# Kernel optimization log

Measured on AMD Instinct MI355X. Metric: run time of the kernel, lower is better.

## Reference

```python
import jax, jax.numpy as jnp
import numpy as np
from jax import lax

B, S, D, F, E, K = 4, 2048, 2048, 8192, 8, 2


def setup_inputs() -> dict:
    key = jax.random.key(0)
    ks = jax.random.split(key, 4)
    sd = 1.0 / np.sqrt(D)
    sf = 1.0 / np.sqrt(F)
    return {
        "hidden_states": jax.random.normal(ks[0], (B, S, D), dtype=jnp.float32),
        "router_w": jax.random.normal(ks[1], (D, E), dtype=jnp.float32) * sd,
        "w1": jax.random.normal(ks[2], (E, D, F), dtype=jnp.float32) * sd,
        "b1": jnp.zeros((E, F), dtype=jnp.float32),
        "w2": jax.random.normal(ks[3], (E, F, D), dtype=jnp.float32) * sf,
        "b2": jnp.zeros((E, D), dtype=jnp.float32),
        "top_k": K,
    }


def reference(hidden_states, router_w, w1, b1, w2, b2, top_k):
    b, s, d = hidden_states.shape
    x = hidden_states.reshape(-1, d)  # [T, D] flat tokens
    # Router: top-k over expert logits, softmax over the selected logits.
    logits = x @ router_w                      # [T, E]
    top_vals, top_idx = lax.top_k(logits, top_k)  # [T, K]
    scores = jax.nn.softmax(top_vals, axis=-1)    # [T, K]

    out = jnp.zeros_like(x)
    n_experts = w1.shape[0]
    for e in range(n_experts):  # fixed small expert count
        # per-token combine weight for this expert (0 if not routed)
        cw = jnp.sum(jnp.where(top_idx == e, scores, 0.0), axis=-1)  # [T]
        h = jax.nn.gelu(x @ w1[e] + b1[e], approximate=False)        # [T, F]
        out = out + cw[:, None] * (h @ w2[e] + b2[e])                # masked combine
    out = out.reshape(b, s, d)
    return out + hidden_states  # use_residual=True
```

## Files before the change

kernel.cpp:

```cpp
#include <hip/hip_runtime.h>

#define T_TOK 8192
#define DIM   2048
#define FFN   8192
#define NE    8
#define TOPK  2

typedef unsigned short ushort_t;
typedef unsigned short ushort8  __attribute__((ext_vector_type(8)));
typedef unsigned short ushort4v __attribute__((ext_vector_type(4)));
typedef short bf16x8 __attribute__((ext_vector_type(8)));
typedef float f32x4  __attribute__((ext_vector_type(4)));

__device__ __forceinline__ ushort_t f2bf(float f) {
  unsigned int u = __float_as_uint(f);
  u += 0x7FFFu + ((u >> 16) & 1u);
  return (ushort_t)(u >> 16);
}
__device__ __forceinline__ float bf2f(ushort_t u) {
  return __uint_as_float(((unsigned int)u) << 16);
}

__device__ __forceinline__ void gload16(const void* g, void* l) {
  __builtin_amdgcn_global_load_lds((const __attribute__((address_space(1))) void*)g,
                                   (__attribute__((address_space(3))) void*)l, 16, 0, 0);
}

__global__ void k_cast(const float* __restrict__ x, ushort_t* __restrict__ xbf) {
  int i = blockIdx.x * blockDim.x + threadIdx.x;
  float4 v = reinterpret_cast<const float4*>(x)[i];
  ushort4v o;
  o.x = f2bf(v.x); o.y = f2bf(v.y); o.z = f2bf(v.z); o.w = f2bf(v.w);
  reinterpret_cast<ushort4v*>(xbf)[i] = o;
}

#define TT 64
__global__ __launch_bounds__(256) void k_wcvt(const float* __restrict__ in,
                                              ushort_t* __restrict__ outp, int R, int C) {
  __shared__ ushort_t t[TT][TT + 8];
  int e = blockIdx.z;
  const float* src = in + (size_t)e * R * C;
  ushort_t* dst = outp + (size_t)e * R * C;
  int r0 = blockIdx.y * TT, c0 = blockIdx.x * TT;
  int tid = threadIdx.x;
  int rr = tid >> 4;
  int c4 = tid & 15;
#pragma unroll
  for (int i = 0; i < 4; i++) {
    int r = rr + i * 16;
    float4 v = *reinterpret_cast<const float4*>(src + (size_t)(r0 + r) * C + c0 + c4 * 4);
    ushort4v p;
    p.x = f2bf(v.x); p.y = f2bf(v.y); p.z = f2bf(v.z); p.w = f2bf(v.w);
    *reinterpret_cast<ushort4v*>(&t[r][c4 * 4]) = p;
  }
  __syncthreads();
  int c = tid >> 2, rs = tid & 3;
  ushort_t tmp[16];
#pragma unroll
  for (int i = 0; i < 16; i++) tmp[i] = t[rs * 16 + i][c];
  ushort8 v0, v1;
#pragma unroll
  for (int i = 0; i < 8; i++) { v0[i] = tmp[i]; v1[i] = tmp[8 + i]; }
  ushort_t* drow = dst + (size_t)(c0 + c) * R + r0 + rs * 16;
  *reinterpret_cast<ushort8*>(drow) = v0;
  *reinterpret_cast<ushort8*>(drow + 8) = v1;
}

__global__ __launch_bounds__(256) void k_router(
    const float* __restrict__ x, const float* __restrict__ rw,
    int* __restrict__ tidx, float* __restrict__ twt, int* __restrict__ counts) {
  int t = blockIdx.x;
  int tid = threadIdx.x;
  int lane = tid & 63, wave = tid >> 6;
  float acc[NE];
#pragma unroll
  for (int e = 0; e < NE; e++) acc[e] = 0.f;
  const float* xr = x + (size_t)t * DIM;
  for (int d = tid; d < DIM; d += 256) {
    float xv = xr[d];
    const float* r = rw + d * NE;
#pragma unroll
    for (int e = 0; e < NE; e++) acc[e] += xv * r[e];
  }
  __shared__ float wsum[4][NE];
#pragma unroll
  for (int e = 0; e < NE; e++) {
    float v = acc[e];
#pragma unroll
    for (int off = 32; off > 0; off >>= 1) v += __shfl_down(v, off);
    if (lane == 0) wsum[wave][e] = v;
  }
  __syncthreads();
  if (tid == 0) {
    float lg[NE];
#pragma unroll
    for (int e = 0; e < NE; e++) lg[e] = wsum[0][e] + wsum[1][e] + wsum[2][e] + wsum[3][e];
    int i0 = 0; float v0 = lg[0];
#pragma unroll
    for (int e = 1; e < NE; e++) if (lg[e] > v0) { v0 = lg[e]; i0 = e; }
    int i1 = -1; float v1 = -3.4e38f;
#pragma unroll
    for (int e = 0; e < NE; e++) if (e != i0 && lg[e] > v1) { v1 = lg[e]; i1 = e; }
    float e1 = expf(v1 - v0);
    float s = 1.f + e1;
    tidx[t * 2 + 0] = i0; tidx[t * 2 + 1] = i1;
    twt[t * 2 + 0] = 1.f / s; twt[t * 2 + 1] = e1 / s;
    atomicAdd(&counts[i0], 1);
    atomicAdd(&counts[i1], 1);
  }
}

__global__ void k_scan(const int* __restrict__ counts, int* __restrict__ offsets) {
  if (threadIdx.x == 0) {
    int s = 0;
    for (int e = 0; e < NE; e++) { offsets[e] = s; s += counts[e]; }
    offsets[NE] = s;
  }
}

__global__ void k_fill(const int* __restrict__ tidx, const float* __restrict__ twt,
                       const int* __restrict__ offsets, int* __restrict__ cursors,
                       int* __restrict__ ltok, float* __restrict__ lwt, int* __restrict__ ppos) {
  int t = blockIdx.x * blockDim.x + threadIdx.x;
  if (t >= T_TOK) return;
#pragma unroll
  for (int k = 0; k < TOPK; k++) {
    int e = tidx[t * 2 + k];
    int pos = atomicAdd(&cursors[e], 1);
    int p = offsets[e] + pos;
    ltok[p] = t;
    lwt[p] = twt[t * 2 + k];
    ppos[t * 2 + k] = p;
  }
}

#define BM 128
#define BN 128
#define BK 32

__global__ __launch_bounds__(256) void k_gemm1(
    const ushort_t* __restrict__ xbf, const ushort_t* __restrict__ w1t, const float* __restrict__ b1,
    const int* __restrict__ counts, const int* __restrict__ offsets,
    const int* __restrict__ ltok, ushort_t* __restrict__ H) {
  int e = blockIdx.z;
  int cnt = counts[e];
  int row0 = blockIdx.y * BM;
  if (row0 >= cnt) return;
  int base = offsets[e];
  int col0 = blockIdx.x * BN;
  const ushort_t* Bt = w1t + (size_t)e * DIM * FFN;

  __shared__ __align__(16) ushort_t As[BM * BK];
  __shared__ __align__(16) ushort_t Bs[BN * BK];

  int tid = threadIdx.x;
  int wave = tid >> 6, lane = tid & 63;
  int wm = wave >> 1, wn = wave & 1;
  int lm = lane & 15, lg = lane >> 4;

  int srow = tid >> 2, seg = tid & 3;
  const ushort_t* asrc[2]; const ushort_t* bsrc[2];
#pragma unroll
  for (int j = 0; j < 2; j++) {
    int ar = min(row0 + j * 64 + srow, cnt - 1);
    asrc[j] = xbf + (size_t)ltok[base + ar] * DIM + seg * 8;
    bsrc[j] = Bt + (size_t)(col0 + j * 64 + srow) * DIM + seg * 8;
  }
  f32x4 acc[4][4];
#pragma unroll
  for (int m = 0; m < 4; m++)
#pragma unroll
    for (int n = 0; n < 4; n++) acc[m][n] = (f32x4){0.f, 0.f, 0.f, 0.f};

  for (int k0 = 0; k0 < DIM; k0 += BK) {
#pragma unroll
    for (int j = 0; j < 2; j++) {
      gload16(asrc[j] + k0, &As[(j * 256 + wave * 64) * 8]);
      gload16(bsrc[j] + k0, &Bs[(j * 256 + wave * 64) * 8]);
    }
    __syncthreads();
    bf16x8 af[4], bfv[4];
#pragma unroll
    for (int m = 0; m < 4; m++)
      af[m] = *reinterpret_cast<const bf16x8*>(&As[(wm * 64 + m * 16 + lm) * BK + lg * 8]);
#pragma unroll
    for (int n = 0; n < 4; n++)
      bfv[n] = *reinterpret_cast<const bf16x8*>(&Bs[(wn * 64 + n * 16 + lm) * BK + lg * 8]);
#pragma unroll
    for (int m = 0; m < 4; m++)
#pragma unroll
      for (int n = 0; n < 4; n++)
        acc[m][n] = __builtin_amdgcn_mfma_f32_16x16x32_bf16(af[m], bfv[n], acc[m][n], 0, 0, 0);
    __syncthreads();
  }
#pragma unroll
  for (int m = 0; m < 4; m++) {
#pragma unroll
    for (int n = 0; n < 4; n++) {
      int f = col0 + wn * 64 + n * 16 + lm;
      float bias = b1[e * FFN + f];
#pragma unroll
      for (int r = 0; r < 4; r++) {
        int row = row0 + wm * 64 + m * 16 + lg * 4 + r;
        if (row < cnt) {
          float v = acc[m][n][r] + bias;
          float g = 0.5f * v * (1.0f + erff(v * 0.70710678118654752f));
          H[(size_t)(base + row) * FFN + f] = f2bf(g);
        }
      }
    }
  }
}

__global__ __launch_bounds__(256) void k_gemm2(
    const ushort_t* __restrict__ H, const ushort_t* __restrict__ w2t, const float* __restrict__ b2,
    const int* __restrict__ counts, const int* __restrict__ offsets,
    const float* __restrict__ lwt, ushort_t* __restrict__ contrib) {
  int e = blockIdx.z;
  int cnt = counts[e];
  int row0 = blockIdx.y * BM;
  if (row0 >= cnt) return;
  int base = offsets[e];
  int col0 = blockIdx.x * BN;
  const ushort_t* Bt = w2t + (size_t)e * DIM * FFN;

  __shared__ __align__(16) ushort_t As[BM * BK];
  __shared__ __align__(16) ushort_t Bs[BN * BK];

  int tid = threadIdx.x;
  int wave = tid >> 6, lane = tid & 63;
  int wm = wave >> 1, wn = wave & 1;
  int lm = lane & 15, lg = lane >> 4;

  int srow = tid >> 2, seg = tid & 3;
  const ushort_t* asrc[2]; const ushort_t* bsrc[2];
#pragma unroll
  for (int j = 0; j < 2; j++) {
    int ar = min(row0 + j * 64 + srow, cnt - 1);
    asrc[j] = H + (size_t)(base + ar) * FFN + seg * 8;
    bsrc[j] = Bt + (size_t)(col0 + j * 64 + srow) * FFN + seg * 8;
  }
  f32x4 acc[4][4];
#pragma unroll
  for (int m = 0; m < 4; m++)
#pragma unroll
    for (int n = 0; n < 4; n++) acc[m][n] = (f32x4){0.f, 0.f, 0.f, 0.f};

  for (int k0 = 0; k0 < FFN; k0 += BK) {
#pragma unroll
    for (int j = 0; j < 2; j++) {
      gload16(asrc[j] + k0, &As[(j * 256 + wave * 64) * 8]);
      gload16(bsrc[j] + k0, &Bs[(j * 256 + wave * 64) * 8]);
    }
    __syncthreads();
    bf16x8 af[4], bfv[4];
#pragma unroll
    for (int m = 0; m < 4; m++)
      af[m] = *reinterpret_cast<const bf16x8*>(&As[(wm * 64 + m * 16 + lm) * BK + lg * 8]);
#pragma unroll
    for (int n = 0; n < 4; n++)
      bfv[n] = *reinterpret_cast<const bf16x8*>(&Bs[(wn * 64 + n * 16 + lm) * BK + lg * 8]);
#pragma unroll
    for (int m = 0; m < 4; m++)
#pragma unroll
      for (int n = 0; n < 4; n++)
        acc[m][n] = __builtin_amdgcn_mfma_f32_16x16x32_bf16(af[m], bfv[n], acc[m][n], 0, 0, 0);
    __syncthreads();
  }
#pragma unroll
  for (int m = 0; m < 4; m++) {
#pragma unroll
    for (int n = 0; n < 4; n++) {
      int d = col0 + wn * 64 + n * 16 + lm;
      float bias = b2[e * DIM + d];
#pragma unroll
      for (int r = 0; r < 4; r++) {
        int row = row0 + wm * 64 + m * 16 + lg * 4 + r;
        if (row < cnt) {
          float v = (acc[m][n][r] + bias) * lwt[base + row];
          contrib[(size_t)(base + row) * DIM + d] = f2bf(v);
        }
      }
    }
  }
}

__global__ void k_combine(const float* __restrict__ x, const ushort_t* __restrict__ contrib,
                          const int* __restrict__ ppos, float* __restrict__ out) {
  int i = blockIdx.x * blockDim.x + threadIdx.x;
  int t = i / (DIM / 4);
  int dq = i % (DIM / 4);
  int p0 = ppos[t * 2 + 0], p1 = ppos[t * 2 + 1];
  float4 xv = reinterpret_cast<const float4*>(x)[i];
  ushort4v c0 = reinterpret_cast<const ushort4v*>(contrib + (size_t)p0 * DIM)[dq];
  ushort4v c1 = reinterpret_cast<const ushort4v*>(contrib + (size_t)p1 * DIM)[dq];
  float4 o;
  o.x = xv.x + bf2f(c0.x) + bf2f(c1.x);
  o.y = xv.y + bf2f(c0.y) + bf2f(c1.y);
  o.z = xv.z + bf2f(c0.z) + bf2f(c1.z);
  o.w = xv.w + bf2f(c0.w) + bf2f(c1.w);
  reinterpret_cast<float4*>(out)[i] = o;
}

extern "C" void kernel_launch(void* const* d_in, const int* in_sizes, int n_in,
                              void* d_out, int out_size, void* d_ws, size_t ws_size,
                              hipStream_t stream) {
  const float* x  = (const float*)d_in[0];
  const float* rw = (const float*)d_in[1];
  const float* w1 = (const float*)d_in[2];
  const float* b1 = (const float*)d_in[3];
  const float* w2 = (const float*)d_in[4];
  const float* b2 = (const float*)d_in[5];
  float* out = (float*)d_out;
  char* ws = (char*)d_ws;

  const size_t MB = 1u << 20;
  int*   counts  = (int*)(ws);
  int*   offsets = (int*)(ws + 64);
  int*   cursors = (int*)(ws + 128);
  int*   tidx    = (int*)(ws + 1 * MB);
  float* twt     = (float*)(ws + 2 * MB);
  int*   ltok    = (int*)(ws + 3 * MB);
  float* lwt     = (float*)(ws + 4 * MB);
  int*   ppos    = (int*)(ws + 5 * MB);
  ushort_t* xbf     = (ushort_t*)(ws + 8 * MB);
  ushort_t* contrib = (ushort_t*)(ws + 8 * MB);
  ushort_t* Hbuf    = (ushort_t*)(ws + 72 * MB);
  ushort_t* w1t     = (ushort_t*)(ws + 328 * MB);
  ushort_t* w2t     = (ushort_t*)(ws + 328 * MB);
  const size_t NEED = 584 * MB;
  if (ws_size < NEED) {
    hipMemsetAsync(d_out, 0, (size_t)out_size * sizeof(float), stream);
    return;
  }

  hipMemsetAsync(ws, 0, 256, stream);
  k_cast<<<dim3((T_TOK * (size_t)DIM / 4) / 256), 256, 0, stream>>>(x, xbf);
  k_router<<<T_TOK, 256, 0, stream>>>(x, rw, tidx, twt, counts);
  k_scan<<<1, 64, 0, stream>>>(counts, offsets);
  k_fill<<<T_TOK / 256, 256, 0, stream>>>(tidx, twt, offsets, cursors, ltok, lwt, ppos);
  k_wcvt<<<dim3(FFN / TT, DIM / TT, NE), 256, 0, stream>>>(w1, w1t, DIM, FFN);
  k_gemm1<<<dim3(FFN / BN, T_TOK / BM, NE), 256, 0, stream>>>(xbf, w1t, b1, counts, offsets, ltok, Hbuf);
  k_wcvt<<<dim3(DIM / TT, FFN / TT, NE), 256, 0, stream>>>(w2, w2t, FFN, DIM);
  k_gemm2<<<dim3(DIM / BN, T_TOK / BM, NE), 256, 0, stream>>>(Hbuf, w2t, b2, counts, offsets, lwt, contrib);
  k_combine<<<dim3((T_TOK * (size_t)DIM / 4) / 256), 256, 0, stream>>>(x, contrib, ppos, out);
}
```

Measured before the change: 2.193 ms.

## Double-buffer LDS in expert GEMMs, swap grid order, faster GELU erf

Both expert GEMM kernels now use two LDS buffers and prefetch the next K-slice while the MFMAs run on the current one, dropping one barrier per iteration. The grid is transposed so the row tiles of one expert (the empty ones exit early) sit in the fast-varying dimension. s_setprio is raised around the MFMA block and launch bounds ask for 4 blocks per CU. The exact erf in GELU is replaced by the Abramowitz-Stegun polynomial with rcp and expf, cutting epilogue cost but adding about 1e-7 absolute erf error, well below bf16 rounding.

```diff
diff --git a/kernel.cpp b/kernel.cpp
--- a/kernel.cpp
+++ b/kernel.cpp
@@ -24,6 +24,20 @@
 __device__ __forceinline__ void gload16(const void* g, void* l) {
   __builtin_amdgcn_global_load_lds((const __attribute__((address_space(1))) void*)g,
                                    (__attribute__((address_space(3))) void*)l, 16, 0, 0);
+}
+
+__device__ __forceinline__ float gelu_exact(float v) {
+  float s = v * 0.70710678118654752f;
+  float a = fabsf(s);
+  float t = __builtin_amdgcn_rcpf(1.0f + 0.3275911f * a);
+  float p = t * (0.254829592f +
+            t * (-0.284496736f +
+            t * (1.421413741f +
+            t * (-1.453152027f +
+            t * 1.061405429f))));
+  float er = 1.0f - p * __expf(-a * a);
+  er = copysignf(er, s);
+  return 0.5f * v * (1.0f + er);
 }
 
 __global__ void k_cast(const float* __restrict__ x, ushort_t* __restrict__ xbf) {
@@ -138,28 +152,28 @@
 #define BN 128
 #define BK 32
 
-__global__ __launch_bounds__(256) void k_gemm1(
+__global__ __launch_bounds__(256, 4) void k_gemm1(
     const ushort_t* __restrict__ xbf, const ushort_t* __restrict__ w1t, const float* __restrict__ b1,
     const int* __restrict__ counts, const int* __restrict__ offsets,
     const int* __restrict__ ltok, ushort_t* __restrict__ H) {
   int e = blockIdx.z;
   int cnt = counts[e];
-  int row0 = blockIdx.y * BM;
+  int row0 = blockIdx.x * BM;
   if (row0 >= cnt) return;
   int base = offsets[e];
-  int col0 = blockIdx.x * BN;
+  int col0 = blockIdx.y * BN;
   const ushort_t* Bt = w1t + (size_t)e * DIM * FFN;
 
-  __shared__ __align__(16) ushort_t As[BM * BK];
-  __shared__ __align__(16) ushort_t Bs[BN * BK];
+  __shared__ __align__(16) ushort_t As[2][BM * BK];
+  __shared__ __align__(16) ushort_t Bs[2][BM * BK];
 
   int tid = threadIdx.x;
   int wave = tid >> 6, lane = tid & 63;
   int wm = wave >> 1, wn = wave & 1;
   int lm = lane & 15, lg = lane >> 4;
 
+  const ushort_t* asrc[2]; const ushort_t* bsrc[2];
   int srow = tid >> 2, seg = tid & 3;
-  const ushort_t* asrc[2]; const ushort_t* bsrc[2];
 #pragma unroll
   for (int j = 0; j < 2; j++) {
     int ar = min(row0 + j * 64 + srow, cnt - 1);
@@ -172,26 +186,37 @@
 #pragma unroll
     for (int n = 0; n < 4; n++) acc[m][n] = (f32x4){0.f, 0.f, 0.f, 0.f};
 
+#pragma unroll
+  for (int j = 0; j < 2; j++) {
+    gload16(asrc[j], &As[0][(j * 256 + wave * 64) * 8]);
+    gload16(bsrc[j], &Bs[0][(j * 256 + wave * 64) * 8]);
+  }
+  __syncthreads();
+  int cur = 0;
   for (int k0 = 0; k0 < DIM; k0 += BK) {
-#pragma unroll
-    for (int j = 0; j < 2; j++) {
-      gload16(asrc[j] + k0, &As[(j * 256 + wave * 64) * 8]);
-      gload16(bsrc[j] + k0, &Bs[(j * 256 + wave * 64) * 8]);
+    if (k0 + BK < DIM) {
+#pragma unroll
+      for (int j = 0; j < 2; j++) {
+        gload16(asrc[j] + k0 + BK, &As[cur ^ 1][(j * 256 + wave * 64) * 8]);
+        gload16(bsrc[j] + k0 + BK, &Bs[cur ^ 1][(j * 256 + wave * 64) * 8]);
+      }
     }
-    __syncthreads();
     bf16x8 af[4], bfv[4];
 #pragma unroll
     for (int m = 0; m < 4; m++)
-      af[m] = *reinterpret_cast<const bf16x8*>(&As[(wm * 64 + m * 16 + lm) * BK + lg * 8]);
+      af[m] = *reinterpret_cast<const bf16x8*>(&As[cur][(wm * 64 + m * 16 + lm) * BK + lg * 8]);
 #pragma unroll
     for (int n = 0; n < 4; n++)
-      bfv[n] = *reinterpret_cast<const bf16x8*>(&Bs[(wn * 64 + n * 16 + lm) * BK + lg * 8]);
+      bfv[n] = *reinterpret_cast<const bf16x8*>(&Bs[cur][(wn * 64 + n * 16 + lm) * BK + lg * 8]);
+    __builtin_amdgcn_s_setprio(1);
 #pragma unroll
     for (int m = 0; m < 4; m++)
 #pragma unroll
       for (int n = 0; n < 4; n++)
         acc[m][n] = __builtin_amdgcn_mfma_f32_16x16x32_bf16(af[m], bfv[n], acc[m][n], 0, 0, 0);
+    __builtin_amdgcn_s_setprio(0);
     __syncthreads();
+    cur ^= 1;
   }
 #pragma unroll
   for (int m = 0; m < 4; m++) {
@@ -204,36 +229,35 @@
         int row = row0 + wm * 64 + m * 16 + lg * 4 + r;
         if (row < cnt) {
           float v = acc[m][n][r] + bias;
-          float g = 0.5f * v * (1.0f + erff(v * 0.70710678118654752f));
-          H[(size_t)(base + row) * FFN + f] = f2bf(g);
+          H[(size_t)(base + row) * FFN + f] = f2bf(gelu_exact(v));
         }
       }
     }
   }
 }
 
-__global__ __launch_bounds__(256) void k_gemm2(
+__global__ __launch_bounds__(256, 4) void k_gemm2(
     const ushort_t* __restrict__ H, const ushort_t* __restrict__ w2t, const float* __restrict__ b2,
     const int* __restrict__ counts, const int* __restrict__ offsets,
     const float* __restrict__ lwt, ushort_t* __restrict__ contrib) {
   int e = blockIdx.z;
   int cnt = counts[e];
-  int row0 = blockIdx.y * BM;
+  int row0 = blockIdx.x * BM;
   if (row0 >= cnt) return;
   int base = offsets[e];
-  int col0 = blockIdx.x * BN;
+  int col0 = blockIdx.y * BN;
   const ushort_t* Bt = w2t + (size_t)e * DIM * FFN;
 
-  __shared__ __align__(16) ushort_t As[BM * BK];
-  __shared__ __align__(16) ushort_t Bs[BN * BK];
+  __shared__ __align__(16) ushort_t As[2][BM * BK];
+  __shared__ __align__(16) ushort_t Bs[2][BM * BK];
 
   int tid = threadIdx.x;
   int wave = tid >> 6, lane = tid & 63;
   int wm = wave >> 1, wn = wave & 1;
   int lm = lane & 15, lg = lane >> 4;
 
+  const ushort_t* asrc[2]; const ushort_t* bsrc[2];
   int srow = tid >> 2, seg = tid & 3;
-  const ushort_t* asrc[2]; const ushort_t* bsrc[2];
 #pragma unroll
   for (int j = 0; j < 2; j++) {
     int ar = min(row0 + j * 64 + srow, cnt - 1);
@@ -246,26 +270,37 @@
 #pragma unroll
     for (int n = 0; n < 4; n++) acc[m][n] = (f32x4){0.f, 0.f, 0.f, 0.f};
 
+#pragma unroll
+  for (int j = 0; j < 2; j++) {
+    gload16(asrc[j], &As[0][(j * 256 + wave * 64) * 8]);
+    gload16(bsrc[j], &Bs[0][(j * 256 + wave * 64) * 8]);
+  }
+  __syncthreads();
+  int cur = 0;
   for (int k0 = 0; k0 < FFN; k0 += BK) {
-#pragma unroll
-    for (int j = 0; j < 2; j++) {
-      gload16(asrc[j] + k0, &As[(j * 256 + wave * 64) * 8]);
-      gload16(bsrc[j] + k0, &Bs[(j * 256 + wave * 64) * 8]);
+    if (k0 + BK < FFN) {
+#pragma unroll
+      for (int j = 0; j < 2; j++) {
+        gload16(asrc[j] + k0 + BK, &As[cur ^ 1][(j * 256 + wave * 64) * 8]);
+        gload16(bsrc[j] + k0 + BK, &Bs[cur ^ 1][(j * 256 + wave * 64) * 8]);
+      }
     }
-    __syncthreads();
     bf16x8 af[4], bfv[4];
 #pragma unroll
     for (int m = 0; m < 4; m++)
-      af[m] = *reinterpret_cast<const bf16x8*>(&As[(wm * 64 + m * 16 + lm) * BK + lg * 8]);
+      af[m] = *reinterpret_cast<const bf16x8*>(&As[cur][(wm * 64 + m * 16 + lm) * BK + lg * 8]);
 #pragma unroll
     for (int n = 0; n < 4; n++)
-      bfv[n] = *reinterpret_cast<const bf16x8*>(&Bs[(wn * 64 + n * 16 + lm) * BK + lg * 8]);
+      bfv[n] = *reinterpret_cast<const bf16x8*>(&Bs[cur][(wn * 64 + n * 16 + lm) * BK + lg * 8]);
+    __builtin_amdgcn_s_setprio(1);
 #pragma unroll
     for (int m = 0; m < 4; m++)
 #pragma unroll
       for (int n = 0; n < 4; n++)
         acc[m][n] = __builtin_amdgcn_mfma_f32_16x16x32_bf16(af[m], bfv[n], acc[m][n], 0, 0, 0);
+    __builtin_amdgcn_s_setprio(0);
     __syncthreads();
+    cur ^= 1;
   }
 #pragma unroll
   for (int m = 0; m < 4; m++) {
@@ -340,8 +375,8 @@
   k_scan<<<1, 64, 0, stream>>>(counts, offsets);
   k_fill<<<T_TOK / 256, 256, 0, stream>>>(tidx, twt, offsets, cursors, ltok, lwt, ppos);
   k_wcvt<<<dim3(FFN / TT, DIM / TT, NE), 256, 0, stream>>>(w1, w1t, DIM, FFN);
-  k_gemm1<<<dim3(FFN / BN, T_TOK / BM, NE), 256, 0, stream>>>(xbf, w1t, b1, counts, offsets, ltok, Hbuf);
+  k_gemm1<<<dim3(T_TOK / BM, FFN / BN, NE), 256, 0, stream>>>(xbf, w1t, b1, counts, offsets, ltok, Hbuf);
   k_wcvt<<<dim3(DIM / TT, FFN / TT, NE), 256, 0, stream>>>(w2, w2t, FFN, DIM);
-  k_gemm2<<<dim3(DIM / BN, T_TOK / BM, NE), 256, 0, stream>>>(Hbuf, w2t, b2, counts, offsets, lwt, contrib);
+  k_gemm2<<<dim3(T_TOK / BM, DIM / BN, NE), 256, 0, stream>>>(Hbuf, w2t, b2, counts, offsets, lwt, contrib);
   k_combine<<<dim3((T_TOK * (size_t)DIM / 4) / 256), 256, 0, stream>>>(x, contrib, ppos, out);
 }
```

After: 3.006 ms. 1.37x slower.

## Double-buffer expert GEMMs with 256x256 tiles, 8 waves, and fast erf GELU

Applied to the files above, without the earlier changes.

Both expert GEMMs now use 256x256 block tiles with 512 threads (8 waves, each computing 128x64), and a double-buffered LDS pipeline. The next K-slice is issued with direct global-to-LDS loads while the current one is computed, with explicit waitcnt and barriers. The grid order is swapped so row tiles vary fastest, and GELU's erff is replaced by an Abramowitz-Stegun polynomial with a hardware reciprocal and fast exp. The aim is to hide global-load latency and raise arithmetic intensity. The cost is heavier register pressure, fewer blocks for the ragged per-expert row counts, and a small accuracy loss in GELU.

```diff
diff --git a/kernel.cpp b/kernel.cpp
--- a/kernel.cpp
+++ b/kernel.cpp
@@ -24,6 +24,20 @@
 __device__ __forceinline__ void gload16(const void* g, void* l) {
   __builtin_amdgcn_global_load_lds((const __attribute__((address_space(1))) void*)g,
                                    (__attribute__((address_space(3))) void*)l, 16, 0, 0);
+}
+
+__device__ __forceinline__ float gelu_exact(float v) {
+  float s = v * 0.70710678118654752f;
+  float a = fabsf(s);
+  float t = __builtin_amdgcn_rcpf(1.0f + 0.3275911f * a);
+  float p = t * (0.254829592f +
+            t * (-0.284496736f +
+            t * (1.421413741f +
+            t * (-1.453152027f +
+            t * 1.061405429f))));
+  float er = 1.0f - p * __expf(-a * a);
+  er = copysignf(er, s);
+  return 0.5f * v * (1.0f + er);
 }
 
 __global__ void k_cast(const float* __restrict__ x, ushort_t* __restrict__ xbf) {
@@ -134,148 +148,165 @@
   }
 }
 
-#define BM 128
-#define BN 128
-#define BK 32
-
-__global__ __launch_bounds__(256) void k_gemm1(
+#define GBM 256
+#define GBN 256
+#define GBK 32
+
+template <int NT>
+__device__ __forceinline__ void gemm_pipe(const ushort_t* a0, const ushort_t* a1,
+                                          const ushort_t* b0, const ushort_t* b1,
+                                          f32x4 (&acc)[8][4]) {
+  __shared__ __align__(16) ushort_t lds[2][2][2][128 * 32];
+  int tid = threadIdx.x;
+  int wid = tid >> 6, lane = tid & 63;
+  int wm = wid >> 2, wn = wid & 3;
+  int lm = lane & 15, lg = lane >> 4;
+
+  const ushort_t* aptr[2] = {a0, a1};
+  const ushort_t* bptr[2] = {b0, b1};
+
+  auto STAGE = [&](int b) {
+#pragma unroll
+    for (int h = 0; h < 2; h++) {
+      gload16(aptr[h], &lds[b][0][h][wid * 512]);
+      gload16(bptr[h], &lds[b][1][h][wid * 512]);
+      aptr[h] += GBK; bptr[h] += GBK;
+    }
+  };
+  auto COMPUTE = [&](int b) {
+    const ushort_t* Ah = &lds[b][0][wm][0];
+    const ushort_t* Bh = &lds[b][1][wn >> 1][0];
+    bf16x8 af[8], bv[4];
+#pragma unroll
+    for (int m = 0; m < 8; m++)
+      af[m] = *reinterpret_cast<const bf16x8*>(&Ah[(m * 16 + lm) * 32 + lg * 8]);
+#pragma unroll
+    for (int n = 0; n < 4; n++)
+      bv[n] = *reinterpret_cast<const bf16x8*>(&Bh[((wn & 1) * 64 + n * 16 + lm) * 32 + lg * 8]);
+#pragma unroll
+    for (int m = 0; m < 8; m++)
+#pragma unroll
+      for (int n = 0; n < 4; n++)
+        acc[m][n] = __builtin_amdgcn_mfma_f32_16x16x32_bf16(af[m], bv[n], acc[m][n], 0, 0, 0);
+  };
+
+  STAGE(0);
+  int cur = 0;
+  for (int t = 0; t < NT - 1; ++t) {
+    STAGE(cur ^ 1);
+    asm volatile("s_waitcnt vmcnt(4)" ::: "memory");
+    __builtin_amdgcn_sched_barrier(0);
+    __builtin_amdgcn_s_barrier();
+    __builtin_amdgcn_sched_barrier(0);
+    COMPUTE(cur);
+    asm volatile("s_waitcnt lgkmcnt(0)" ::: "memory");
+    __builtin_amdgcn_sched_barrier(0);
+    __builtin_amdgcn_s_barrier();
+    __builtin_amdgcn_sched_barrier(0);
+    cur ^= 1;
+  }
+  asm volatile("s_waitcnt vmcnt(0)" ::: "memory");
+  __builtin_amdgcn_sched_barrier(0);
+  __builtin_amdgcn_s_barrier();
+  __builtin_amdgcn_sched_barrier(0);
+  COMPUTE(cur);
+}
+
+__global__ __launch_bounds__(512, 2) void k_gemm1(
     const ushort_t* __restrict__ xbf, const ushort_t* __restrict__ w1t, const float* __restrict__ b1,
     const int* __restrict__ counts, const int* __restrict__ offsets,
     const int* __restrict__ ltok, ushort_t* __restrict__ H) {
   int e = blockIdx.z;
   int cnt = counts[e];
-  int row0 = blockIdx.y * BM;
+  int row0 = blockIdx.x * GBM;
   if (row0 >= cnt) return;
   int base = offsets[e];
-  int col0 = blockIdx.x * BN;
+  int col0 = blockIdx.y * GBN;
   const ushort_t* Bt = w1t + (size_t)e * DIM * FFN;
 
-  __shared__ __align__(16) ushort_t As[BM * BK];
-  __shared__ __align__(16) ushort_t Bs[BN * BK];
-
-  int tid = threadIdx.x;
-  int wave = tid >> 6, lane = tid & 63;
-  int wm = wave >> 1, wn = wave & 1;
+  int tid = threadIdx.x;
+  int hrow = tid >> 2, slot = tid & 3;
+  const ushort_t* aptr[2]; const ushort_t* bptr[2];
+#pragma unroll
+  for (int h = 0; h < 2; h++) {
+    int R = h * 128 + hrow;
+    int ar = min(row0 + R, cnt - 1);
+    aptr[h] = xbf + (size_t)ltok[base + ar] * DIM + slot * 8;
+    bptr[h] = Bt + (size_t)(col0 + R) * DIM + slot * 8;
+  }
+
+  f32x4 acc[8][4];
+#pragma unroll
+  for (int m = 0; m < 8; m++)
+#pragma unroll
+    for (int n = 0; n < 4; n++) acc[m][n] = (f32x4){0.f, 0.f, 0.f, 0.f};
+
+  gemm_pipe<DIM / GBK>(aptr[0], aptr[1], bptr[0], bptr[1], acc);
+
+  int wid = tid >> 6, lane = tid & 63;
+  int wm = wid >> 2, wn = wid & 3;
   int lm = lane & 15, lg = lane >> 4;
-
-  int srow = tid >> 2, seg = tid & 3;
-  const ushort_t* asrc[2]; const ushort_t* bsrc[2];
-#pragma unroll
-  for (int j = 0; j < 2; j++) {
-    int ar = min(row0 + j * 64 + srow, cnt - 1);
-    asrc[j] = xbf + (size_t)ltok[base + ar] * DIM + seg * 8;
-    bsrc[j] = Bt + (size_t)(col0 + j * 64 + srow) * DIM + seg * 8;
-  }
-  f32x4 acc[4][4];
-#pragma unroll
-  for (int m = 0; m < 4; m++)
-#pragma unroll
-    for (int n = 0; n < 4; n++) acc[m][n] = (f32x4){0.f, 0.f, 0.f, 0.f};
-
-  for (int k0 = 0; k0 < DIM; k0 += BK) {
-#pragma unroll
-    for (int j = 0; j < 2; j++) {
-      gload16(asrc[j] + k0, &As[(j * 256 + wave * 64) * 8]);
-      gload16(bsrc[j] + k0, &Bs[(j * 256 + wave * 64) * 8]);
-    }
-    __syncthreads();
-    bf16x8 af[4], bfv[4];
-#pragma unroll
-    for (int m = 0; m < 4; m++)
-      af[m] = *reinterpret_cast<const bf16x8*>(&As[(wm * 64 + m * 16 + lm) * BK + lg * 8]);
-#pragma unroll
-    for (int n = 0; n < 4; n++)
-      bfv[n] = *reinterpret_cast<const bf16x8*>(&Bs[(wn * 64 + n * 16 + lm) * BK + lg * 8]);
-#pragma unroll
-    for (int m = 0; m < 4; m++)
-#pragma unroll
-      for (int n = 0; n < 4; n++)
-        acc[m][n] = __builtin_amdgcn_mfma_f32_16x16x32_bf16(af[m], bfv[n], acc[m][n], 0, 0, 0);
-    __syncthreads();
-  }
-#pragma unroll
-  for (int m = 0; m < 4; m++) {
+#pragma unroll
+  for (int m = 0; m < 8; m++) {
 #pragma unroll
     for (int n = 0; n < 4; n++) {
       int f = col0 + wn * 64 + n * 16 + lm;
       float bias = b1[e * FFN + f];
 #pragma unroll
       for (int r = 0; r < 4; r++) {
-        int row = row0 + wm * 64 + m * 16 + lg * 4 + r;
+        int row = row0 + wm * 128 + m * 16 + lg * 4 + r;
         if (row < cnt) {
           float v = acc[m][n][r] + bias;
-          float g = 0.5f * v * (1.0f + erff(v * 0.70710678118654752f));
-          H[(size_t)(base + row) * FFN + f] = f2bf(g);
+          H[(size_t)(base + row) * FFN + f] = f2bf(gelu_exact(v));
         }
       }
     }
   }
 }
 
-__global__ __launch_bounds__(256) void k_gemm2(
+__global__ __launch_bounds__(512, 2) void k_gemm2(
     const ushort_t* __restrict__ H, const ushort_t* __restrict__ w2t, const float* __restrict__ b2,
     const int* __restrict__ counts, const int* __restrict__ offsets,
     const float* __restrict__ lwt, ushort_t* __restrict__ contrib) {
   int e = blockIdx.z;
   int cnt = counts[e];
-  int row0 = blockIdx.y * BM;
+  int row0 = blockIdx.x * GBM;
   if (row0 >= cnt) return;
   int base = offsets[e];
-  int col0 = blockIdx.x * BN;
+  int col0 = blockIdx.y * GBN;
   const ushort_t* Bt = w2t + (size_t)e * DIM * FFN;
 
-  __shared__ __align__(16) ushort_t As[BM * BK];
-  __shared__ __align__(16) ushort_t Bs[BN * BK];
-
-  int tid = threadIdx.x;
-  int wave = tid >> 6, lane = tid & 63;
-  int wm = wave >> 1, wn = wave & 1;
+  int tid = threadIdx.x;
+  int hrow = tid >> 2, slot = tid & 3;
+  const ushort_t* aptr[2]; const ushort_t* bptr[2];
+#pragma unroll
+  for (int h = 0; h < 2; h++) {
+    int R = h * 128 + hrow;
+    int ar = min(row0 + R, cnt - 1);
+    aptr[h] = H + (size_t)(base + ar) * FFN + slot * 8;
+    bptr[h] = Bt + (size_t)(col0 + R) * FFN + slot * 8;
+  }
+
+  f32x4 acc[8][4];
+#pragma unroll
+  for (int m = 0; m < 8; m++)
+#pragma unroll
+    for (int n = 0; n < 4; n++) acc[m][n] = (f32x4){0.f, 0.f, 0.f, 0.f};
+
+  gemm_pipe<FFN / GBK>(aptr[0], aptr[1], bptr[0], bptr[1], acc);
+
+  int wid = tid >> 6, lane = tid & 63;
+  int wm = wid >> 2, wn = wid & 3;
   int lm = lane & 15, lg = lane >> 4;
-
-  int srow = tid >> 2, seg = tid & 3;
-  const ushort_t* asrc[2]; const ushort_t* bsrc[2];
-#pragma unroll
-  for (int j = 0; j < 2; j++) {
-    int ar = min(row0 + j * 64 + srow, cnt - 1);
-    asrc[j] = H + (size_t)(base + ar) * FFN + seg * 8;
-    bsrc[j] = Bt + (size_t)(col0 + j * 64 + srow) * FFN + seg * 8;
-  }
-  f32x4 acc[4][4];
-#pragma unroll
-  for (int m = 0; m < 4; m++)
-#pragma unroll
-    for (int n = 0; n < 4; n++) acc[m][n] = (f32x4){0.f, 0.f, 0.f, 0.f};
-
-  for (int k0 = 0; k0 < FFN; k0 += BK) {
-#pragma unroll
-    for (int j = 0; j < 2; j++) {
-      gload16(asrc[j] + k0, &As[(j * 256 + wave * 64) * 8]);
-      gload16(bsrc[j] + k0, &Bs[(j * 256 + wave * 64) * 8]);
-    }
-    __syncthreads();
-    bf16x8 af[4], bfv[4];
-#pragma unroll
-    for (int m = 0; m < 4; m++)
-      af[m] = *reinterpret_cast<const bf16x8*>(&As[(wm * 64 + m * 16 + lm) * BK + lg * 8]);
-#pragma unroll
-    for (int n = 0; n < 4; n++)
-      bfv[n] = *reinterpret_cast<const bf16x8*>(&Bs[(wn * 64 + n * 16 + lm) * BK + lg * 8]);
-#pragma unroll
-    for (int m = 0; m < 4; m++)
-#pragma unroll
-      for (int n = 0; n < 4; n++)
-        acc[m][n] = __builtin_amdgcn_mfma_f32_16x16x32_bf16(af[m], bfv[n], acc[m][n], 0, 0, 0);
-    __syncthreads();
-  }
-#pragma unroll
-  for (int m = 0; m < 4; m++) {
+#pragma unroll
+  for (int m = 0; m < 8; m++) {
 #pragma unroll
     for (int n = 0; n < 4; n++) {
       int d = col0 + wn * 64 + n * 16 + lm;
       float bias = b2[e * DIM + d];
 #pragma unroll
       for (int r = 0; r < 4; r++) {
-        int row = row0 + wm * 64 + m * 16 + lg * 4 + r;
+        int row = row0 + wm * 128 + m * 16 + lg * 4 + r;
         if (row < cnt) {
           float v = (acc[m][n][r] + bias) * lwt[base + row];
           contrib[(size_t)(base + row) * DIM + d] = f2bf(v);
@@ -340,8 +371,8 @@
   k_scan<<<1, 64, 0, stream>>>(counts, offsets);
   k_fill<<<T_TOK / 256, 256, 0, stream>>>(tidx, twt, offsets, cursors, ltok, lwt, ppos);
   k_wcvt<<<dim3(FFN / TT, DIM / TT, NE), 256, 0, stream>>>(w1, w1t, DIM, FFN);
-  k_gemm1<<<dim3(FFN / BN, T_TOK / BM, NE), 256, 0, stream>>>(xbf, w1t, b1, counts, offsets, ltok, Hbuf);
+  k_gemm1<<<dim3(T_TOK / GBM, FFN / GBN, NE), 512, 0, stream>>>(xbf, w1t, b1, counts, offsets, ltok, Hbuf);
   k_wcvt<<<dim3(DIM / TT, FFN / TT, NE), 256, 0, stream>>>(w2, w2t, FFN, DIM);
-  k_gemm2<<<dim3(DIM / BN, T_TOK / BM, NE), 256, 0, stream>>>(Hbuf, w2t, b2, counts, offsets, lwt, contrib);
+  k_gemm2<<<dim3(T_TOK / GBM, DIM / GBN, NE), 512, 0, stream>>>(Hbuf, w2t, b2, counts, offsets, lwt, contrib);
   k_combine<<<dim3((T_TOK * (size_t)DIM / 4) / 256), 256, 0, stream>>>(x, contrib, ppos, out);
 }
```

Measured after the change: 5.504 ms. +150.9%, slower.
